# Kernel tuning notes

Measured on AMD Instinct MI355X. Metric: run time of the kernel, lower is better.

The kernel has to match this reference:

```python
import jax, jax.numpy as jnp
import numpy as np

N_NODES = 100000
N_EDGES = 3200000
D_IN, D_HID, D_OUT = 128, 128, 40


def _sage_conv(x, src, dst, W_l, W_r, b, counts):
    # mean aggregation of neighbor (source) features at destination nodes
    agg = jax.ops.segment_sum(x[src], dst, num_segments=N_NODES)  # [N, d]
    agg = agg / counts  # mean (isolated nodes stay zero via clamped counts)
    # PyG SAGEConv: out = lin_l(aggr) + lin_r(x_root); bias lives in lin_l
    return agg @ W_l + x @ W_r + b


def setup_inputs() -> dict:
    key = jax.random.key(0)
    ks = jax.random.split(key, 8)
    x = jax.random.normal(ks[0], (N_NODES, D_IN), dtype=jnp.float32)
    edge_index = jax.random.randint(ks[1], (2, N_EDGES), 0, N_NODES, dtype=jnp.int64)
    s1 = 1.0 / np.sqrt(D_IN)
    s2 = 1.0 / np.sqrt(D_HID)
    return {
        "x": x,
        "edge_index": edge_index,
        "W1_l": jax.random.uniform(ks[2], (D_IN, D_HID), jnp.float32, -s1, s1),
        "W1_r": jax.random.uniform(ks[3], (D_IN, D_HID), jnp.float32, -s1, s1),
        "b1": jnp.zeros((D_HID,), jnp.float32),
        "W2_l": jax.random.uniform(ks[4], (D_HID, D_OUT), jnp.float32, -s2, s2),
        "W2_r": jax.random.uniform(ks[5], (D_HID, D_OUT), jnp.float32, -s2, s2),
        "b2": jnp.zeros((D_OUT,), jnp.float32),
    }


def reference(x, edge_index, W1_l, W1_r, b1, W2_l, W2_r, b2):
    src, dst = edge_index[0], edge_index[1]
    # in-degree per destination node, clamped to avoid div-by-zero
    deg = jax.ops.segment_sum(jnp.ones((N_EDGES,), jnp.float32), dst, num_segments=N_NODES)
    counts = jnp.maximum(deg, 1.0)[:, None]  # [N, 1]
    h = jax.nn.relu(_sage_conv(x, src, dst, W1_l, W1_r, b1, counts))
    h = _sage_conv(h, src, dst, W2_l, W2_r, b2, counts)
    return jax.nn.log_softmax(h, axis=1)
```

## Files before the change

### kernel.cpp

```cpp
#include <hip/hip_runtime.h>
#include <hip/hip_bf16.h>
#include <hip/hip_fp8.h>
#include <math.h>

#define N_NODES 100000
#define D_IN    128
#define D_HID   128
#define D_OUT   40
#define NBUCK   391
#define CHUNK   8192
#define STAGECAP 12160
#define CAST_BLOCKS_1K 1563


using short8  = __attribute__((ext_vector_type(8))) short;
using float4v = __attribute__((ext_vector_type(4))) float;
using floatx2 = __attribute__((ext_vector_type(2))) float;

__device__ __forceinline__ unsigned short f2b(float f) {
    __hip_bfloat16 b = __float2bfloat16(f);
    return *(unsigned short*)&b;
}
__device__ __forceinline__ unsigned packb(float a, float b) {
    return (unsigned)f2b(a) | ((unsigned)f2b(b) << 16);
}

__device__ __forceinline__ unsigned char f2q(float f) {
    __hip_fp8_e4m3 v(f);
    return *(unsigned char*)&v;
}
template <int SEL>
__device__ __forceinline__ float q2f(unsigned u) {
#if __has_builtin(__builtin_amdgcn_cvt_f32_fp8)
    return __builtin_amdgcn_cvt_f32_fp8((int)u, SEL);
#else
    unsigned char b = (u >> (SEL * 8)) & 0xff;
    __hip_fp8_e4m3 v;
    *(unsigned char*)&v = b;
    return (float)v;
#endif
}
template <bool HI>
__device__ __forceinline__ floatx2 pkcvt(unsigned u) {
#if __has_builtin(__builtin_amdgcn_cvt_pk_f32_fp8)
    return __builtin_amdgcn_cvt_pk_f32_fp8((int)u, HI);
#else
    floatx2 r;
    if constexpr (HI) { r[0] = q2f<2>(u); r[1] = q2f<3>(u); }
    else              { r[0] = q2f<0>(u); r[1] = q2f<1>(u); }
    return r;
#endif
}

__device__ __forceinline__ long long edge_at(const void* ei, int is64, long long idx) {
    if (is64) return ((const long long*)ei)[idx];
    return (long long)((const int*)ei)[idx];
}

__global__ __launch_bounds__(1024) void mega_kernel(const void* __restrict__ ei,
                                                    unsigned* __restrict__ slab,
                                                    unsigned* __restrict__ lofs,
                                                    long long E, int npb,
                                                    const float* __restrict__ x,
                                                    unsigned short* __restrict__ xb,
                                                    unsigned char* __restrict__ xq,
                                                    const float* __restrict__ W1l,
                                                    const float* __restrict__ W1r,
                                                    const float* __restrict__ W2l,
                                                    const float* __restrict__ W2r,
                                                    unsigned short* __restrict__ wp1,
                                                    unsigned short* __restrict__ wp2) {
    __shared__ unsigned hist[NBUCK];
    __shared__ unsigned lstart[NBUCK];
    __shared__ unsigned wsum[16];
    __shared__ unsigned rec[CHUNK];
    __shared__ int sflag[1];

    const int blk = blockIdx.x;
    const int tid = threadIdx.x;

    if (blk >= npb) {
        const int cb = blk - npb;
        if (cb < CAST_BLOCKS_1K) {
            long long i = ((long long)cb * 1024 + tid) * 8;
            if (i >= (long long)N_NODES * 128) return;
            float4 a = *(const float4*)&x[i];
            float4 c = *(const float4*)&x[i + 4];
            ushort4 o0, o1;
            o0.x = f2b(a.x); o0.y = f2b(a.y); o0.z = f2b(a.z); o0.w = f2b(a.w);
            o1.x = f2b(c.x); o1.y = f2b(c.y); o1.z = f2b(c.z); o1.w = f2b(c.w);
            *(ushort4*)&xb[i] = o0;
            *(ushort4*)&xb[i + 4] = o1;
            uint2 p;
            p.x = (unsigned)f2q(a.x) | ((unsigned)f2q(a.y) << 8)
                | ((unsigned)f2q(a.z) << 16) | ((unsigned)f2q(a.w) << 24);
            p.y = (unsigned)f2q(c.x) | ((unsigned)f2q(c.y) << 8)
                | ((unsigned)f2q(c.z) << 16) | ((unsigned)f2q(c.w) << 24);
            *(uint2*)&xq[i] = p;
        } else {
            int t = (cb - CAST_BLOCKS_1K) * 1024 + tid;
            if (t < 4096) {
                int lane = t & 63;
                int ks = (t >> 6) & 7;
                int ct = t >> 9;
                int n = ct * 16 + (lane & 15);
                int kr = (lane >> 4) * 8;
                unsigned short v[8];
#pragma unroll
                for (int j = 0; j < 8; ++j) {
                    int k = ks * 32 + kr + j;
                    float f = (k < 128) ? W1l[k * 128 + n] : W1r[(k - 128) * 128 + n];
                    v[j] = f2b(f);
                }
                ushort4 o0 = {v[0], v[1], v[2], v[3]};
                ushort4 o1 = {v[4], v[5], v[6], v[7]};
                *(ushort4*)&wp1[t * 8] = o0;
                *(ushort4*)&wp1[t * 8 + 4] = o1;
            } else if (t < 4096 + 1280) {
                int u = t - 4096;
                int lane = u & 63;
                int ks = (u >> 6) & 3;
                int ct = u >> 8;
                int n = ct * 16 + (lane & 15);
                int kr = (lane >> 4) * 8;
                unsigned short v[8];
#pragma unroll
                for (int j = 0; j < 8; ++j) {
                    int k = ks * 32 + kr + j;
                    float f = (n < 40) ? W2l[k * 40 + n] : W2r[k * 40 + (n - 40)];
                    v[j] = f2b(f);
                }
                ushort4 o0 = {v[0], v[1], v[2], v[3]};
                ushort4 o1 = {v[4], v[5], v[6], v[7]};
                *(ushort4*)&wp2[u * 8] = o0;
                *(ushort4*)&wp2[u * 8 + 4] = o1;
            }
        }
        return;
    }

    const int lane = tid & 63;
    const int w = tid >> 6;

    if (w == 0) {
        const int* e32 = (const int*)ei;
        int ok = 1;
#pragma unroll
        for (int k = 0; k < 4; ++k) {
            if (e32[2 * (lane * 4 + k) + 1] != 0) ok = 0;
        }
        int all0 = __all(ok);
        if (lane == 0) sflag[0] = all0;
    }
    if (tid < NBUCK) hist[tid] = 0;
    __syncthreads();
    const int is64 = sflag[0];

    const long long cb64 = (long long)blk * CHUNK;
    const unsigned n = (unsigned)(((E - cb64) < (long long)CHUNK) ? (E - cb64) : CHUNK);

    unsigned esrc[CHUNK / 1024], edst[CHUNK / 1024];
#pragma unroll
    for (int j = 0; j < CHUNK / 1024; ++j) {
        unsigned e = j * 1024 + tid;
        if (e < n) {
            esrc[j] = (unsigned)edge_at(ei, is64, cb64 + e);
            edst[j] = (unsigned)edge_at(ei, is64, E + cb64 + e);
            atomicAdd(&hist[edst[j] >> 8], 1u);
        }
    }
    __syncthreads();

    {
        unsigned v0 = (tid < NBUCK) ? hist[tid] : 0u;
        unsigned xx = v0;
#pragma unroll
        for (int off = 1; off < 64; off <<= 1) {
            unsigned t = __shfl_up(xx, off);
            if (lane >= off) xx += t;
        }
        if (lane == 63) wsum[w] = xx;
        __syncthreads();
        if (w == 0) {
            unsigned y = (lane < 16) ? wsum[lane] : 0u;
#pragma unroll
            for (int off = 1; off < 16; off <<= 1) {
                unsigned t = __shfl_up(y, off);
                if (lane >= off) y += t;
            }
            if (lane < 16) wsum[lane] = y;
        }
        __syncthreads();
        unsigned pre = (w > 0) ? wsum[w - 1] : 0u;
        if (tid < NBUCK) {
            unsigned ex = xx + pre - v0;
            lstart[tid] = ex;
            lofs[(unsigned)tid * (unsigned)npb + (unsigned)blk] = ex;
            hist[tid] = 0;
        }
        if (tid == 0) lofs[(unsigned)NBUCK * (unsigned)npb + (unsigned)blk] = n;
    }
    __syncthreads();

#pragma unroll
    for (int j = 0; j < CHUNK / 1024; ++j) {
        unsigned e = j * 1024 + tid;
        if (e < n) {
            unsigned d = edst[j];
            unsigned b = d >> 8;
            unsigned loc = atomicAdd(&hist[b], 1u);
            rec[lstart[b] + loc] = ((d & 255u) << 17) | esrc[j];
        }
    }
    __syncthreads();

#pragma unroll
    for (int j = 0; j < CHUNK / 1024; ++j) {
        unsigned i = j * 1024 + tid;
        if (i < n) slab[(unsigned)blk * (unsigned)CHUNK + i] = rec[i];
    }
}

__global__ __launch_bounds__(256) void build_kernel(const unsigned* __restrict__ slab,
                                                    const unsigned* __restrict__ lofs,
                                                    int npb,
                                                    unsigned* __restrict__ deg,
                                                    float* __restrict__ invc,
                                                    unsigned* __restrict__ row_start,
                                                    int* __restrict__ csr) {
    __shared__ unsigned rstart[NBUCK];
    __shared__ unsigned rcnt[NBUCK];
    __shared__ unsigned pofs[NBUCK];
    __shared__ unsigned redlds[4];
    __shared__ unsigned wsum2[4];
    __shared__ unsigned cnt[256];
    __shared__ unsigned stage[STAGECAP];

    const int tid = threadIdx.x;
    const int lane = tid & 63;
    const int w = tid >> 6;
    const int b = blockIdx.x;
    const int nb = b << 8;

    unsigned psum = 0;
    for (int p = tid; p < npb; p += 256) {
        unsigned lo = lofs[(unsigned)b * (unsigned)npb + (unsigned)p];
        unsigned hi = lofs[(unsigned)(b + 1) * (unsigned)npb + (unsigned)p];
        rstart[p] = lo;
        rcnt[p] = hi - lo;
        psum += lo;
    }
#pragma unroll
    for (int off = 32; off >= 1; off >>= 1) psum += __shfl_xor(psum, off);
    if (lane == 0) redlds[w] = psum;
    __syncthreads();
    const unsigned es = redlds[0] + redlds[1] + redlds[2] + redlds[3];

    if (w == 0) {
        unsigned carry = 0;
        for (int r = 0; r < (npb + 63) / 64; ++r) {
            int p = r * 64 + lane;
            unsigned c = (p < npb) ? rcnt[p] : 0u;
            unsigned x = c;
#pragma unroll
            for (int off = 1; off < 64; off <<= 1) {
                unsigned t = __shfl_up(x, off);
                if (lane >= off) x += t;
            }
            if (p < npb) pofs[p] = x - c + carry;
            carry += __shfl(x, 63);
        }
    }
    __syncthreads();
    const unsigned n = pofs[npb - 1] + rcnt[npb - 1];

    for (int p = tid; p < npb; p += 256) {
        unsigned src = (unsigned)p * (unsigned)CHUNK + rstart[p];
        unsigned dst = pofs[p];
        unsigned c = rcnt[p];
        for (unsigned i = 0; i < c; ++i)
            stage[dst + i] = slab[src + i];
    }
    __syncthreads();

    cnt[tid] = 0;
    __syncthreads();
    for (unsigned i = tid; i < n; i += 256) {
        atomicAdd(&cnt[stage[i] >> 17], 1u);
    }
    __syncthreads();
    unsigned v = cnt[tid];
    unsigned x = v;
#pragma unroll
    for (int off = 1; off < 64; off <<= 1) {
        unsigned t = __shfl_up(x, off);
        if (lane >= off) x += t;
    }
    if (lane == 63) wsum2[w] = x;
    __syncthreads();
    unsigned pre = 0;
#pragma unroll
    for (int k = 0; k < 4; ++k) if (k < w) pre += wsum2[k];
    unsigned ex = x + pre - v;
    int node = nb + tid;
    if (node < N_NODES) {
        deg[node] = v;
        invc[node] = 1.0f / fmaxf((float)v, 1.0f);
        row_start[node] = es + ex;
    }
    __syncthreads();
    cnt[tid] = ex;
    __syncthreads();
    for (unsigned i = tid; i < n; i += 256) {
        unsigned pr = stage[i];
        unsigned d = pr >> 17;
        unsigned pos = es + atomicAdd(&cnt[d], 1u);
        csr[pos] = (int)(pr & 0x1FFFFu);
    }
}

__global__ __launch_bounds__(256) void gather_fp8_kernel(const unsigned char* __restrict__ featq,
                                                         const int* __restrict__ csr,
                                                         const unsigned* __restrict__ row_start,
                                                         const unsigned* __restrict__ deg,
                                                         const float* __restrict__ invc,
                                                         unsigned short* __restrict__ aggb) {
    const int wave = threadIdx.x >> 6;
    const int lane = threadIdx.x & 63;
    const int node = blockIdx.x * 4 + wave;
    if (node >= N_NODES) return;

    const unsigned start = row_start[node];
    const unsigned cnt = deg[node];
    const int s = lane >> 4;
    const unsigned cgo = (unsigned)((lane & 15) * 8);

    floatx2 acc[4];
#pragma unroll
    for (int k = 0; k < 4; ++k) acc[k] = (floatx2){0.f, 0.f};

    for (unsigned base = 0; base < cnt; base += 64) {
        unsigned rem = cnt - base;
        if (rem > 64u) rem = 64u;
        int nid = (lane < (int)rem) ? csr[start + base + lane] : 0;
        for (unsigned j = 0; j < rem; j += 8) {
            uint2 u0 = {0u, 0u}, u1 = {0u, 0u};
            unsigned i0 = j + s;
            unsigned i1 = j + 4 + s;
            int s0 = __shfl(nid, (int)(i0 & 63));
            int s1 = __shfl(nid, (int)(i1 & 63));
            if (i0 < rem) u0 = *(const uint2*)&featq[((unsigned)s0 << 7) + cgo];
            if (i1 < rem) u1 = *(const uint2*)&featq[((unsigned)s1 << 7) + cgo];
            acc[0] += pkcvt<false>(u0.x); acc[1] += pkcvt<true>(u0.x);
            acc[2] += pkcvt<false>(u0.y); acc[3] += pkcvt<true>(u0.y);
            acc[0] += pkcvt<false>(u1.x); acc[1] += pkcvt<true>(u1.x);
            acc[2] += pkcvt<false>(u1.y); acc[3] += pkcvt<true>(u1.y);
        }
    }

#pragma unroll
    for (int k = 0; k < 4; ++k) {
        acc[k][0] += __shfl_xor(acc[k][0], 16);
        acc[k][1] += __shfl_xor(acc[k][1], 16);
        acc[k][0] += __shfl_xor(acc[k][0], 32);
        acc[k][1] += __shfl_xor(acc[k][1], 32);
    }

    if (lane < 16) {
        const float ic = invc[node];
        uint4 o;
        o.x = packb(acc[0][0] * ic, acc[0][1] * ic);
        o.y = packb(acc[1][0] * ic, acc[1][1] * ic);
        o.z = packb(acc[2][0] * ic, acc[2][1] * ic);
        o.w = packb(acc[3][0] * ic, acc[3][1] * ic);
        *(uint4*)&aggb[(unsigned)node * 128u + cgo] = o;
    }
}

__global__ __launch_bounds__(256) void gemm12_kernel(const unsigned short* __restrict__ aggb,
                                                     const unsigned short* __restrict__ xb,
                                                     const unsigned short* __restrict__ wp1,
                                                     const float* __restrict__ b1,
                                                     const unsigned short* __restrict__ wp2,
                                                     const float* __restrict__ b2,
                                                     unsigned char* __restrict__ pq,
                                                     float* __restrict__ q) {
    __shared__ unsigned short sh[64][136];
    const int wave = threadIdx.x >> 6;
    const int lane = threadIdx.x & 63;
    const int row0 = blockIdx.x * 64 + wave * 16;
    const unsigned abase = (unsigned)(row0 + (lane & 15)) * 128u + (unsigned)((lane >> 4) * 8);

    float4v acc[8];
#pragma unroll
    for (int ct = 0; ct < 8; ++ct) acc[ct] = (float4v){0.f, 0.f, 0.f, 0.f};

#pragma unroll
    for (int ks = 0; ks < 8; ++ks) {
        union { uint4 u; short8 s; } af;
        if (ks < 4) af.u = *(const uint4*)&aggb[abase + ks * 32];
        else        af.u = *(const uint4*)&xb[abase + (ks - 4) * 32];
#pragma unroll
        for (int ct = 0; ct < 8; ++ct) {
            union { uint4 u; short8 s; } bf;
            bf.u = *(const uint4*)&wp1[((ct * 8 + ks) * 64 + lane) * 8];
            acc[ct] = __builtin_amdgcn_mfma_f32_16x16x32_bf16(af.s, bf.s, acc[ct], 0, 0, 0);
        }
    }

    const int lrow0 = wave * 16 + (lane >> 4) * 4;
    const int ccol = lane & 15;
#pragma unroll
    for (int ct = 0; ct < 8; ++ct) {
        const int col = ct * 16 + ccol;
        const float bv = b1[col];
#pragma unroll
        for (int r = 0; r < 4; ++r)
            sh[lrow0 + r][col] = f2b(fmaxf(acc[ct][r] + bv, 0.0f));
    }

    const unsigned short* aptr = &sh[wave * 16 + (lane & 15)][(lane >> 4) * 8];

    float4v acc2[5];
#pragma unroll
    for (int ct = 0; ct < 5; ++ct) acc2[ct] = (float4v){0.f, 0.f, 0.f, 0.f};

#pragma unroll
    for (int ks = 0; ks < 4; ++ks) {
        union { uint4 u; short8 s; } af;
        af.u = *(const uint4*)&aptr[ks * 32];
#pragma unroll
        for (int ct = 0; ct < 5; ++ct) {
            union { uint4 u; short8 s; } bf;
            bf.u = *(const uint4*)&wp2[((ct * 4 + ks) * 64 + lane) * 8];
            acc2[ct] = __builtin_amdgcn_mfma_f32_16x16x32_bf16(af.s, bf.s, acc2[ct], 0, 0, 0);
        }
    }

    const int crow0 = row0 + (lane >> 4) * 4;
#pragma unroll
    for (int ct = 0; ct < 5; ++ct) {
        const int col = ct * 16 + ccol;
#pragma unroll
        for (int r = 0; r < 4; ++r) {
            int row = crow0 + r;
            if (row < N_NODES) {
                if (col < D_OUT) {
                    pq[(unsigned)row * 40u + (unsigned)col] = f2q(acc2[ct][r]);
                } else {
                    q[(unsigned)row * 40u + (unsigned)(col - D_OUT)] = acc2[ct][r] + b2[col - D_OUT];
                }
            }
        }
    }
}

__global__ __launch_bounds__(256) void gather40_kernel(const unsigned char* __restrict__ pq,
                                                       const float* __restrict__ q,
                                                       const int* __restrict__ csr,
                                                       const unsigned* __restrict__ row_start,
                                                       const unsigned* __restrict__ deg,
                                                       const float* __restrict__ invc,
                                                       float* __restrict__ out) {
    __shared__ float sm[4][40];
    const int wave = threadIdx.x >> 6;
    const int lane = threadIdx.x & 63;
    const int node = blockIdx.x * 4 + wave;
    if (node >= N_NODES) return;

    const unsigned start = row_start[node];
    const unsigned cnt = deg[node];
    const int s = lane / 10;
    const int cg = lane % 10;
    const unsigned cgo = (unsigned)(cg * 4);
    const bool gactive = s < 6;

    floatx2 a01 = (floatx2){0.f, 0.f}, a23 = (floatx2){0.f, 0.f};

    for (unsigned base = 0; base < cnt; base += 64) {
        unsigned rem = cnt - base;
        if (rem > 64u) rem = 64u;
        int nid = (lane < (int)rem) ? csr[start + base + lane] : 0;
        for (unsigned j = 0; j < rem; j += 24) {
            unsigned u[4];
#pragma unroll
            for (int t = 0; t < 4; ++t) {
                unsigned idx = j + t * 6 + s;
                int sid = __shfl(nid, (int)(idx & 63));
                bool valid = gactive && (idx < rem);
                u[t] = valid ? *(const unsigned*)&pq[(unsigned)sid * 40u + cgo] : 0u;
            }
#pragma unroll
            for (int t = 0; t < 4; ++t) {
                a01 += pkcvt<false>(u[t]);
                a23 += pkcvt<true>(u[t]);
            }
        }
    }

    float a0 = a01[0], a1 = a01[1], a2 = a23[0], a3 = a23[1];
    {
        float t0, t1, t2, t3;
        t0 = __shfl(a0, lane + 30); t1 = __shfl(a1, lane + 30);
        t2 = __shfl(a2, lane + 30); t3 = __shfl(a3, lane + 30);
        if (lane < 30) { a0 += t0; a1 += t1; a2 += t2; a3 += t3; }
        t0 = __shfl(a0, lane + 20); t1 = __shfl(a1, lane + 20);
        t2 = __shfl(a2, lane + 20); t3 = __shfl(a3, lane + 20);
        if (lane < 10) { a0 += t0; a1 += t1; a2 += t2; a3 += t3; }
        t0 = __shfl(a0, lane + 10); t1 = __shfl(a1, lane + 10);
        t2 = __shfl(a2, lane + 10); t3 = __shfl(a3, lane + 10);
        if (lane < 10) { a0 += t0; a1 += t1; a2 += t2; a3 += t3; }
    }
    if (lane < 10) {
        sm[wave][cg * 4 + 0] = a0;
        sm[wave][cg * 4 + 1] = a1;
        sm[wave][cg * 4 + 2] = a2;
        sm[wave][cg * 4 + 3] = a3;
    }
    const bool active = lane < D_OUT;
    float v = active ? (sm[wave][active ? lane : 0] * invc[node]
                        + q[(unsigned)node * 40u + (unsigned)(active ? lane : 0)])
                     : -__builtin_huge_valf();
    float m = v;
#pragma unroll
    for (int off = 32; off >= 1; off >>= 1) m = fmaxf(m, __shfl_xor(m, off));
    float e = active ? expf(v - m) : 0.0f;
    float ssum = e;
#pragma unroll
    for (int off = 32; off >= 1; off >>= 1) ssum += __shfl_xor(ssum, off);
    float ls = logf(ssum);
    if (active) out[(unsigned)node * 40u + (unsigned)lane] = v - m - ls;
}

extern "C" void kernel_launch(void* const* d_in, const int* in_sizes, int n_in,
                              void* d_out, int out_size, void* d_ws, size_t ws_size,
                              hipStream_t stream) {
    const float* x   = (const float*)d_in[0];
    const void*  ei  = d_in[1];
    const float* W1l = (const float*)d_in[2];
    const float* W1r = (const float*)d_in[3];
    const float* b1  = (const float*)d_in[4];
    const float* W2l = (const float*)d_in[5];
    const float* W2r = (const float*)d_in[6];
    const float* b2  = (const float*)d_in[7];
    float* out = (float*)d_out;

    const long long E = (long long)in_sizes[1] / 2;
    const int NPB = (int)((E + CHUNK - 1) / CHUNK);

    char* ws = (char*)d_ws;
    unsigned* deg       = (unsigned*)(ws + 16384);
    float*    invc      = (float*)(ws + 416384);
    unsigned* row_start = (unsigned*)(ws + 816384);
    int*      csr       = (int*)(ws + 1216384);
    unsigned short* xb  = (unsigned short*)(ws + 14016384);
    unsigned short* aggb= (unsigned short*)(ws + 39616384);
    unsigned* slab      = (unsigned*)(ws + 39616384);
    unsigned short* wp1 = (unsigned short*)(ws + 65216384);
    unsigned short* wp2 = (unsigned short*)(ws + 65281920);
    unsigned char*  pq  = (unsigned char*)(ws + 65310720);
    float*    q         = (float*)(ws + 69310720);
    unsigned char*  xq  = (unsigned char*)(ws + 90910720);
    unsigned* lofs      = (unsigned*)(ws + 103710720);

    mega_kernel<<<NPB + CAST_BLOCKS_1K + 6, 1024, 0, stream>>>(
        ei, slab, lofs, E, NPB,
        x, xb, xq, W1l, W1r, W2l, W2r, wp1, wp2);

    build_kernel<<<NBUCK, 256, 0, stream>>>(slab, lofs, NPB, deg, invc, row_start, csr);

    gather_fp8_kernel<<<(N_NODES + 3) / 4, 256, 0, stream>>>(xq, csr, row_start, deg, invc, aggb);
    gemm12_kernel<<<(N_NODES + 63) / 64, 256, 0, stream>>>(aggb, xb, wp1, b1, wp2, b2, pq, q);

    gather40_kernel<<<(N_NODES + 3) / 4, 256, 0, stream>>>(pq, q, csr, row_start, deg, invc, out);
}
```

Baseline: 297.0 us.

## Widen CSR build blocks to 1024 threads and use 8-byte loads in final gather

The CSR build kernel moves from 256 to 1024 threads per block. Its slab-to-stage copy now gives each partition to a 32-lane group instead of a single thread walking the segment serially, which spreads that copy across many more threads and makes it coalesced. The 40-wide layer-2 gather now has each lane load 8 bytes (8 fp8 values) for 12 neighbor slots across 5 lanes, rather than 4 bytes for 6 slots across 10 lanes, which halves the load instructions per edge. The trade-off is a different shuffle-reduction tree, and 1024-thread blocks may lower occupancy for the build kernel, whose prefix scan still runs on only the first 256 threads.

Result: slower. 311.7 us (+5.0%).

```diff
diff --git a/kernel.cpp b/kernel.cpp
--- a/kernel.cpp
+++ b/kernel.cpp
@@ -221,17 +221,17 @@
     }
 }
 
-__global__ __launch_bounds__(256) void build_kernel(const unsigned* __restrict__ slab,
-                                                    const unsigned* __restrict__ lofs,
-                                                    int npb,
-                                                    unsigned* __restrict__ deg,
-                                                    float* __restrict__ invc,
-                                                    unsigned* __restrict__ row_start,
-                                                    int* __restrict__ csr) {
+__global__ __launch_bounds__(1024) void build_kernel(const unsigned* __restrict__ slab,
+                                                     const unsigned* __restrict__ lofs,
+                                                     int npb,
+                                                     unsigned* __restrict__ deg,
+                                                     float* __restrict__ invc,
+                                                     unsigned* __restrict__ row_start,
+                                                     int* __restrict__ csr) {
     __shared__ unsigned rstart[NBUCK];
     __shared__ unsigned rcnt[NBUCK];
     __shared__ unsigned pofs[NBUCK];
-    __shared__ unsigned redlds[4];
+    __shared__ unsigned redlds[16];
     __shared__ unsigned wsum2[4];
     __shared__ unsigned cnt[256];
     __shared__ unsigned stage[STAGECAP];
@@ -243,7 +243,7 @@
     const int nb = b << 8;
 
     unsigned psum = 0;
-    for (int p = tid; p < npb; p += 256) {
+    for (int p = tid; p < npb; p += 1024) {
         unsigned lo = lofs[(unsigned)b * (unsigned)npb + (unsigned)p];
         unsigned hi = lofs[(unsigned)(b + 1) * (unsigned)npb + (unsigned)p];
         rstart[p] = lo;
@@ -254,7 +254,9 @@
     for (int off = 32; off >= 1; off >>= 1) psum += __shfl_xor(psum, off);
     if (lane == 0) redlds[w] = psum;
     __syncthreads();
-    const unsigned es = redlds[0] + redlds[1] + redlds[2] + redlds[3];
+    unsigned es = 0;
+#pragma unroll
+    for (int k = 0; k < 16; ++k) es += redlds[k];
 
     if (w == 0) {
         unsigned carry = 0;
@@ -274,44 +276,52 @@
     __syncthreads();
     const unsigned n = pofs[npb - 1] + rcnt[npb - 1];
 
-    for (int p = tid; p < npb; p += 256) {
-        unsigned src = (unsigned)p * (unsigned)CHUNK + rstart[p];
-        unsigned dst = pofs[p];
-        unsigned c = rcnt[p];
-        for (unsigned i = 0; i < c; ++i)
-            stage[dst + i] = slab[src + i];
-    }
-    __syncthreads();
-
-    cnt[tid] = 0;
-    __syncthreads();
-    for (unsigned i = tid; i < n; i += 256) {
+    {
+        const int sg = tid >> 5;
+        const int sl = tid & 31;
+        for (int p = sg; p < npb; p += 32) {
+            unsigned src = (unsigned)p * (unsigned)CHUNK + rstart[p];
+            unsigned dst = pofs[p];
+            unsigned c = rcnt[p];
+            for (unsigned i = sl; i < c; i += 32)
+                stage[dst + i] = slab[src + i];
+        }
+    }
+    __syncthreads();
+
+    if (tid < 256) cnt[tid] = 0;
+    __syncthreads();
+    for (unsigned i = tid; i < n; i += 1024) {
         atomicAdd(&cnt[stage[i] >> 17], 1u);
     }
     __syncthreads();
-    unsigned v = cnt[tid];
-    unsigned x = v;
-#pragma unroll
-    for (int off = 1; off < 64; off <<= 1) {
-        unsigned t = __shfl_up(x, off);
-        if (lane >= off) x += t;
-    }
-    if (lane == 63) wsum2[w] = x;
-    __syncthreads();
-    unsigned pre = 0;
-#pragma unroll
-    for (int k = 0; k < 4; ++k) if (k < w) pre += wsum2[k];
-    unsigned ex = x + pre - v;
-    int node = nb + tid;
-    if (node < N_NODES) {
-        deg[node] = v;
-        invc[node] = 1.0f / fmaxf((float)v, 1.0f);
-        row_start[node] = es + ex;
-    }
-    __syncthreads();
-    cnt[tid] = ex;
-    __syncthreads();
-    for (unsigned i = tid; i < n; i += 256) {
+    unsigned v = 0, x = 0;
+    if (tid < 256) {
+        v = cnt[tid];
+        x = v;
+#pragma unroll
+        for (int off = 1; off < 64; off <<= 1) {
+            unsigned t = __shfl_up(x, off);
+            if (lane >= off) x += t;
+        }
+        if (lane == 63) wsum2[w] = x;
+    }
+    __syncthreads();
+    if (tid < 256) {
+        unsigned pre = 0;
+#pragma unroll
+        for (int k = 0; k < 4; ++k) if (k < w) pre += wsum2[k];
+        unsigned ex = x + pre - v;
+        int node = nb + tid;
+        if (node < N_NODES) {
+            deg[node] = v;
+            invc[node] = 1.0f / fmaxf((float)v, 1.0f);
+            row_start[node] = es + ex;
+        }
+        cnt[tid] = ex;
+    }
+    __syncthreads();
+    for (unsigned i = tid; i < n; i += 1024) {
         unsigned pr = stage[i];
         unsigned d = pr >> 17;
         unsigned pos = es + atomicAdd(&cnt[d], 1u);
@@ -470,52 +480,62 @@
 
     const unsigned start = row_start[node];
     const unsigned cnt = deg[node];
-    const int s = lane / 10;
-    const int cg = lane % 10;
-    const unsigned cgo = (unsigned)(cg * 4);
-    const bool gactive = s < 6;
-
-    floatx2 a01 = (floatx2){0.f, 0.f}, a23 = (floatx2){0.f, 0.f};
+    const int s = lane / 5;
+    const int cg = lane % 5;
+    const unsigned cgo = (unsigned)(cg * 8);
+    const bool gactive = s < 12;
+
+    floatx2 acc[4];
+#pragma unroll
+    for (int k = 0; k < 4; ++k) acc[k] = (floatx2){0.f, 0.f};
 
     for (unsigned base = 0; base < cnt; base += 64) {
         unsigned rem = cnt - base;
         if (rem > 64u) rem = 64u;
         int nid = (lane < (int)rem) ? csr[start + base + lane] : 0;
         for (unsigned j = 0; j < rem; j += 24) {
-            unsigned u[4];
-#pragma unroll
-            for (int t = 0; t < 4; ++t) {
-                unsigned idx = j + t * 6 + s;
+            uint2 u[2];
+#pragma unroll
+            for (int t = 0; t < 2; ++t) {
+                unsigned idx = j + (unsigned)(t * 12 + s);
                 int sid = __shfl(nid, (int)(idx & 63));
                 bool valid = gactive && (idx < rem);
-                u[t] = valid ? *(const unsigned*)&pq[(unsigned)sid * 40u + cgo] : 0u;
+                u[t] = (uint2){0u, 0u};
+                if (valid) u[t] = *(const uint2*)&pq[(unsigned)sid * 40u + cgo];
             }
 #pragma unroll
-            for (int t = 0; t < 4; ++t) {
-                a01 += pkcvt<false>(u[t]);
-                a23 += pkcvt<true>(u[t]);
+            for (int t = 0; t < 2; ++t) {
+                acc[0] += pkcvt<false>(u[t].x); acc[1] += pkcvt<true>(u[t].x);
+                acc[2] += pkcvt<false>(u[t].y); acc[3] += pkcvt<true>(u[t].y);
             }
         }
     }
 
-    float a0 = a01[0], a1 = a01[1], a2 = a23[0], a3 = a23[1];
-    {
-        float t0, t1, t2, t3;
-        t0 = __shfl(a0, lane + 30); t1 = __shfl(a1, lane + 30);
-        t2 = __shfl(a2, lane + 30); t3 = __shfl(a3, lane + 30);
-        if (lane < 30) { a0 += t0; a1 += t1; a2 += t2; a3 += t3; }
-        t0 = __shfl(a0, lane + 20); t1 = __shfl(a1, lane + 20);
-        t2 = __shfl(a2, lane + 20); t3 = __shfl(a3, lane + 20);
-        if (lane < 10) { a0 += t0; a1 += t1; a2 += t2; a3 += t3; }
-        t0 = __shfl(a0, lane + 10); t1 = __shfl(a1, lane + 10);
-        t2 = __shfl(a2, lane + 10); t3 = __shfl(a3, lane + 10);
-        if (lane < 10) { a0 += t0; a1 += t1; a2 += t2; a3 += t3; }
-    }
-    if (lane < 10) {
-        sm[wave][cg * 4 + 0] = a0;
-        sm[wave][cg * 4 + 1] = a1;
-        sm[wave][cg * 4 + 2] = a2;
-        sm[wave][cg * 4 + 3] = a3;
+#pragma unroll
+    for (int k = 0; k < 4; ++k) {
+        float t0 = __shfl(acc[k][0], lane + 30);
+        float t1 = __shfl(acc[k][1], lane + 30);
+        if (lane < 30) { acc[k][0] += t0; acc[k][1] += t1; }
+    }
+#pragma unroll
+    for (int k = 0; k < 4; ++k) {
+        float t0 = __shfl(acc[k][0], lane + 15);
+        float t1 = __shfl(acc[k][1], lane + 15);
+        if (lane < 15) { acc[k][0] += t0; acc[k][1] += t1; }
+    }
+#pragma unroll
+    for (int k = 0; k < 4; ++k) {
+        float a0 = __shfl(acc[k][0], lane + 5);
+        float a1 = __shfl(acc[k][1], lane + 5);
+        float b0 = __shfl(acc[k][0], lane + 10);
+        float b1 = __shfl(acc[k][1], lane + 10);
+        if (lane < 5) { acc[k][0] += a0 + b0; acc[k][1] += a1 + b1; }
+    }
+    if (lane < 5) {
+        float4 f0 = {acc[0][0], acc[0][1], acc[1][0], acc[1][1]};
+        float4 f1 = {acc[2][0], acc[2][1], acc[3][0], acc[3][1]};
+        *(float4*)&sm[wave][cg * 8] = f0;
+        *(float4*)&sm[wave][cg * 8 + 4] = f1;
     }
     const bool active = lane < D_OUT;
     float v = active ? (sm[wave][active ? lane : 0] * invc[node]
@@ -567,7 +587,7 @@
         ei, slab, lofs, E, NPB,
         x, xb, xq, W1l, W1r, W2l, W2r, wp1, wp2);
 
-    build_kernel<<<NBUCK, 256, 0, stream>>>(slab, lofs, NPB, deg, invc, row_start, csr);
+    build_kernel<<<NBUCK, 1024, 0, stream>>>(slab, lofs, NPB, deg, invc, row_start, csr);
 
     gather_fp8_kernel<<<(N_NODES + 3) / 4, 256, 0, stream>>>(xq, csr, row_start, deg, invc, aggb);
     gemm12_kernel<<<(N_NODES + 63) / 64, 256, 0, stream>>>(aggb, xb, wp1, b1, wp2, b2, pq, q);
```
